# Optimization experiments

Hardware: AMD Instinct MI355X
Metric: run time of the kernel (lower is better)

Reference implementation:

```python
import jax, jax.numpy as jnp
import numpy as np

D_MODEL, D_K, D_V = 1024, 64, 64
B, S = 2, 4096
NEG = 1e9


def setup_inputs() -> dict:
    key = jax.random.key(0)
    ks = jax.random.split(key, 10)
    Q = jax.random.normal(ks[0], (B, S, D_MODEL), dtype=jnp.float32)
    K = jax.random.normal(ks[1], (B, S, D_MODEL), dtype=jnp.float32)
    V = jax.random.normal(ks[2], (B, S, D_MODEL), dtype=jnp.float32)
    mask = jax.random.randint(ks[3], (B, S, S), 0, 2, dtype=jnp.int32)
    sc = 1.0 / np.sqrt(D_MODEL)
    Wq = jax.random.normal(ks[4], (D_K, D_MODEL), dtype=jnp.float32) * sc
    bq = jnp.zeros((D_K,), dtype=jnp.float32)
    Wk = jax.random.normal(ks[5], (D_K, D_MODEL), dtype=jnp.float32) * sc
    bk = jnp.zeros((D_K,), dtype=jnp.float32)
    Wv = jax.random.normal(ks[6], (D_V, D_MODEL), dtype=jnp.float32) * sc
    bv = jnp.zeros((D_V,), dtype=jnp.float32)
    return {"Q": Q, "K": K, "V": V, "mask": mask,
            "Wq": Wq, "bq": bq, "Wk": Wk, "bk": bk, "Wv": Wv, "bv": bv}


def reference(Q, K, V, mask, Wq, bq, Wk, bk, Wv, bv):
    # Linear projections: q,k -> [B,S,d_k], v -> [B,S,d_v]
    q = jnp.einsum('bsm,km->bsk', Q, Wq) + bq
    k = jnp.einsum('bsm,km->bsk', K, Wk) + bk
    v = jnp.einsum('bsm,vm->bsv', V, Wv) + bv
    # Scaled dot-product scores [B,S,S]
    x = jnp.einsum('bqk,bsk->bqs', q, k) / jnp.sqrt(jnp.float32(D_K))
    m = mask.astype(x.dtype)
    x = x * m - NEG * (1.0 - m)
    x = jax.nn.softmax(x, axis=2)
    y = jnp.einsum('bqs,bsv->bqv', x, v)
    return y
```

## Files before the change

### kernel.cpp

```cpp
#include <hip/hip_runtime.h>

typedef unsigned short u16;
typedef unsigned long long u64;
typedef __bf16 bf16x8 __attribute__((ext_vector_type(8)));
typedef float f32x4 __attribute__((ext_vector_type(4)));
typedef int i32x4 __attribute__((ext_vector_type(4)));

#define MFMA16(a, b, c) __builtin_amdgcn_mfma_f32_16x16x32_bf16((a), (b), (c), 0, 0, 0)

__device__ __forceinline__ bf16x8 ld8(const u16* p) {
    return *reinterpret_cast<const bf16x8*>(p);
}

__device__ __forceinline__ unsigned pk2(float a, float b) {
    unsigned short ua = __builtin_bit_cast(unsigned short, (__bf16)a);
    unsigned short ub = __builtin_bit_cast(unsigned short, (__bf16)b);
    return (unsigned)ua | ((unsigned)ub << 16);
}

__device__ __forceinline__ f32x4 ntf4(const float* p) {
    return __builtin_nontemporal_load(reinterpret_cast<const f32x4*>(p));
}
__device__ __forceinline__ i32x4 nti4(const int* p) {
    return __builtin_nontemporal_load(reinterpret_cast<const i32x4*>(p));
}

__global__ __launch_bounds__(256) void wcvt_kernel(
    const float* __restrict__ Wq, const float* __restrict__ Wk,
    const float* __restrict__ Wv, u16* __restrict__ wb)
{
    const int t = blockIdx.x * 256 + threadIdx.x;
    const int mat = t >> 13;
    const int idx = (t & 8191) * 8;
    const float* src = (mat == 0) ? Wq : (mat == 1) ? Wk : Wv;
    const f32x4 a = *(const f32x4*)(src + idx);
    const f32x4 b = *(const f32x4*)(src + idx + 4);
    uint4 o;
    o.x = pk2(a[0], a[1]); o.y = pk2(a[2], a[3]);
    o.z = pk2(b[0], b[1]); o.w = pk2(b[2], b[3]);
    *reinterpret_cast<uint4*>(wb + (size_t)mat * 65536 + idx) = o;
}

__global__ __launch_bounds__(256) void fused_kernel(
    const float* __restrict__ Q, const float* __restrict__ K, const float* __restrict__ V,
    const float* __restrict__ bq, const float* __restrict__ bk, const float* __restrict__ bv,
    const u16* __restrict__ wb, const int* __restrict__ mask,
    u16* __restrict__ qb, u16* __restrict__ kb, u16* __restrict__ vtb,
    u64* __restrict__ bits)
{
    __shared__ uint2 xlds[16][256];
    const int lane = threadIdx.x & 63, w = threadIdx.x >> 6;

    if (blockIdx.x >= 1536) {
        const int row = (blockIdx.x - 1536) * 4 + w;
        const int* mp = mask + (size_t)row * 4096 + lane * 4;
        u64* op = bits + (size_t)row * 64;

        i32x4 h0[8], h1[8];
        #pragma unroll
        for (int j = 0; j < 8; ++j) h0[j] = nti4(mp + j * 256);
        #pragma unroll
        for (int j = 0; j < 8; ++j) h1[j] = nti4(mp + 2048 + j * 256);

        u64 mine0 = 0, mine1 = 0;
        #pragma unroll
        for (int j = 0; j < 8; ++j) {
            const u64 b0 = __ballot(h0[j][0] != 0);
            const u64 b1 = __ballot(h0[j][1] != 0);
            const u64 b2 = __ballot(h0[j][2] != 0);
            const u64 b3 = __ballot(h0[j][3] != 0);
            if (lane == j * 4 + 0) mine0 = b0;
            if (lane == j * 4 + 1) mine0 = b1;
            if (lane == j * 4 + 2) mine0 = b2;
            if (lane == j * 4 + 3) mine0 = b3;
            const u64 c0 = __ballot(h1[j][0] != 0);
            const u64 c1 = __ballot(h1[j][1] != 0);
            const u64 c2 = __ballot(h1[j][2] != 0);
            const u64 c3 = __ballot(h1[j][3] != 0);
            if (lane == j * 4 + 0) mine1 = c0;
            if (lane == j * 4 + 1) mine1 = c1;
            if (lane == j * 4 + 2) mine1 = c2;
            if (lane == j * 4 + 3) mine1 = c3;
        }
        if (lane < 32) { op[lane] = mine0; op[32 + lane] = mine1; }
        return;
    }

    const int mat  = blockIdx.x >> 9;
    const int tile = blockIdx.x & 511;
    const int r0   = tile * 16;
    const int t    = threadIdx.x;
    const float* X = (mat == 0) ? Q : (mat == 1) ? K : V;

    f32x4 st[16];
    const float* xp = X + (size_t)r0 * 1024 + t * 4;
    #pragma unroll
    for (int i = 0; i < 16; ++i) st[i] = ntf4(xp + i * 1024);

    #pragma unroll
    for (int i = 0; i < 16; ++i) {
        xlds[i][(((t >> 1) ^ (i & 7)) << 1) | (t & 1)] =
            make_uint2(pk2(st[i][0], st[i][1]), pk2(st[i][2], st[i][3]));
    }
    __syncthreads();

    const int c = lane & 15, g = lane >> 4;
    const u16* wp = wb + (size_t)mat * 65536 + (size_t)(w * 16 + c) * 1024 + g * 8;

    f32x4 acc = {};
    #pragma unroll
    for (int kk = 0; kk < 32; ++kk) {
        const bf16x8 a = ld8((const u16*)&xlds[c][((kk * 4 + g) ^ (c & 7)) << 1]);
        const bf16x8 wf = ld8(wp + kk * 32);
        if (mat < 2) acc = MFMA16(a, wf, acc);
        else         acc = MFMA16(wf, a, acc);
    }

    if (mat < 2) {
        const float* bias = (mat == 0) ? bq : bk;
        u16* dst = (mat == 0) ? qb : kb;
        const float bz = bias[w * 16 + c];
        #pragma unroll
        for (int r = 0; r < 4; ++r) {
            dst[(size_t)(r0 + g * 4 + r) * 64 + w * 16 + c] =
                __builtin_bit_cast(u16, (__bf16)(acc[r] + bz));
        }
    } else {
        const int sg = r0 + c;
        const int bidx = sg >> 12, sin = sg & 4095;
        #pragma unroll
        for (int r = 0; r < 4; ++r) {
            const int dv = w * 16 + g * 4 + r;
            vtb[(size_t)(bidx * 64 + dv) * 4096 + sin] =
                __builtin_bit_cast(u16, (__bf16)(acc[r] + bv[dv]));
        }
    }
}

__global__ __launch_bounds__(256) void attn_kernel(
    const u64* __restrict__ bits, const u16* __restrict__ qb,
    const u16* __restrict__ kb, const u16* __restrict__ vtb,
    float* __restrict__ pacc, float* __restrict__ pm, float* __restrict__ pl)
{
    __shared__ uint2 plds[4][128];
    const int lane = threadIdx.x & 63, w = threadIdx.x >> 6;
    const int c = lane & 15, g = lane >> 4;
    const int gw    = blockIdx.x * 4 + w;
    const int strip = gw >> 3;
    const int chunk = gw & 7;
    const int b     = strip >> 8;
    const int q0    = (strip & 255) * 16;
    const int sBase = chunk * 512;
    const float SSC = 0.18033688011112042f;

    const u16* qrow = qb + (size_t)((b << 12) + q0 + c) * 64 + g * 8;
    const bf16x8 qf0 = ld8(qrow);
    const bf16x8 qf1 = ld8(qrow + 32);

    const u16* kfp = kb  + (((size_t)b << 12) + sBase + c) * 64 + g * 8;
    const u16* vfp = vtb + (size_t)(b * 64 + c) * 4096 + sBase + g * 8;

    const u64* bp = bits + (size_t)((b << 12) + q0 + c) * 64 + chunk * 8;
    const u64 Wd0 = bp[0], Wd1 = bp[1], Wd2 = bp[2], Wd3 = bp[3];
    const u64 Wd4 = bp[4], Wd5 = bp[5], Wd6 = bp[6], Wd7 = bp[7];

    f32x4 acc0 = {}, acc1 = {}, acc2 = {}, acc3 = {};
    const f32x4 zf = {};
    float m_run = -__builtin_inff(), l_run = 0.f;

    bf16x8 k00 = ld8(kfp),            k01 = ld8(kfp + 32);
    bf16x8 k10 = ld8(kfp + 16 * 64),  k11 = ld8(kfp + 16 * 64 + 32);

    #pragma unroll
    for (int half = 0; half < 2; ++half) {
        const u64 Wr0 = half ? Wd4 : Wd0;
        const u64 Wr1 = half ? Wd5 : Wd1;
        const u64 Wr2 = half ? Wd6 : Wd2;
        const u64 Wr3 = half ? Wd7 : Wd3;
        #pragma unroll 1
        for (int it2 = 0; it2 < 8; ++it2) {
            const int it = half * 8 + it2;

            const u16* vp = vfp + it * 32;
            const bf16x8 v0 = ld8(vp);
            const bf16x8 v1 = ld8(vp + 16 * 4096);
            const bf16x8 v2 = ld8(vp + 32 * 4096);
            const bf16x8 v3 = ld8(vp + 48 * 4096);

            f32x4 d0 = MFMA16(k00, qf0, zf);
            d0 = MFMA16(k01, qf1, d0);
            f32x4 d1 = MFMA16(k10, qf0, zf);
            d1 = MFMA16(k11, qf1, d1);

            const int no = (it < 15) ? (it + 1) * 2048 : it * 2048;
            k00 = ld8(kfp + no);            k01 = ld8(kfp + no + 32);
            k10 = ld8(kfp + no + 16 * 64);  k11 = ld8(kfp + no + 16 * 64 + 32);

            const int sh = it2 * 8 + g;
            const unsigned t0 = (unsigned)(Wr0 >> sh);
            const unsigned t1 = (unsigned)(Wr1 >> sh);
            const unsigned t2 = (unsigned)(Wr2 >> sh);
            const unsigned t3 = (unsigned)(Wr3 >> sh);

            const float x0 = (t0 & 1u)  ? d0[0] * SSC : -1e9f;
            const float x1 = (t1 & 1u)  ? d0[1] * SSC : -1e9f;
            const float x2 = (t2 & 1u)  ? d0[2] * SSC : -1e9f;
            const float x3 = (t3 & 1u)  ? d0[3] * SSC : -1e9f;
            const float x4 = (t0 & 16u) ? d1[0] * SSC : -1e9f;
            const float x5 = (t1 & 16u) ? d1[1] * SSC : -1e9f;
            const float x6 = (t2 & 16u) ? d1[2] * SSC : -1e9f;
            const float x7 = (t3 & 16u) ? d1[3] * SSC : -1e9f;

            float tm = fmaxf(fmaxf(fmaxf(x0, x1), fmaxf(x2, x3)),
                             fmaxf(fmaxf(x4, x5), fmaxf(x6, x7)));
            tm = fmaxf(tm, __shfl_xor(tm, 16));
            tm = fmaxf(tm, __shfl_xor(tm, 32));
            const float m_new = fmaxf(m_run, tm);
            const float f = exp2f(m_run - m_new);

            const float p0 = exp2f(x0 - m_new), p1 = exp2f(x1 - m_new);
            const float p2 = exp2f(x2 - m_new), p3 = exp2f(x3 - m_new);
            const float p4 = exp2f(x4 - m_new), p5 = exp2f(x5 - m_new);
            const float p6 = exp2f(x6 - m_new), p7 = exp2f(x7 - m_new);
            float rs = ((p0 + p1) + (p2 + p3)) + ((p4 + p5) + (p6 + p7));
            rs += __shfl_xor(rs, 16);
            rs += __shfl_xor(rs, 32);
            l_run = l_run * f + rs;
            m_run = m_new;

            plds[w][c * 8 + ( g      ^ (c & 7))] = make_uint2(pk2(p0, p1), pk2(p2, p3));
            plds[w][c * 8 + ((g + 4) ^ (c & 7))] = make_uint2(pk2(p4, p5), pk2(p6, p7));

            if (__any(f < 1.0f)) {
                const float f0 = __shfl(f, g * 4 + 0);
                const float f1 = __shfl(f, g * 4 + 1);
                const float f2 = __shfl(f, g * 4 + 2);
                const float f3 = __shfl(f, g * 4 + 3);
                acc0[0] *= f0; acc0[1] *= f1; acc0[2] *= f2; acc0[3] *= f3;
                acc1[0] *= f0; acc1[1] *= f1; acc1[2] *= f2; acc1[3] *= f3;
                acc2[0] *= f0; acc2[1] *= f1; acc2[2] *= f2; acc2[3] *= f3;
                acc3[0] *= f0; acc3[1] *= f1; acc3[2] *= f2; acc3[3] *= f3;
            }

            union { uint2 u[2]; bf16x8 v; } pa;
            pa.u[0] = plds[w][c * 8 + ((2 * g    ) ^ (c & 7))];
            pa.u[1] = plds[w][c * 8 + ((2 * g + 1) ^ (c & 7))];

            acc0 = MFMA16(pa.v, v0, acc0);
            acc1 = MFMA16(pa.v, v1, acc1);
            acc2 = MFMA16(pa.v, v2, acc2);
            acc3 = MFMA16(pa.v, v3, acc3);
        }
    }

    const size_t pidx = (size_t)(strip * 8 + chunk) * 16;
    #pragma unroll
    for (int r = 0; r < 4; ++r) {
        const size_t row = pidx + g * 4 + r;
        pacc[row * 64 +  0 + c] = acc0[r];
        pacc[row * 64 + 16 + c] = acc1[r];
        pacc[row * 64 + 32 + c] = acc2[r];
        pacc[row * 64 + 48 + c] = acc3[r];
    }
    if (lane < 16) {
        pm[pidx + c] = m_run;
        pl[pidx + c] = l_run;
    }
}

__global__ __launch_bounds__(256) void comb_kernel(
    const float* __restrict__ pacc, const float* __restrict__ pm,
    const float* __restrict__ pl, float* __restrict__ out)
{
    const int t = blockIdx.x * 256 + threadIdx.x;
    const int r = t >> 6, dv = t & 63;
    const int strip = r >> 4, qi = r & 15;
    const int base = strip * 128 + qi;
    float mv[8];
    float M = -__builtin_inff();
    #pragma unroll
    for (int cc = 0; cc < 8; ++cc) { mv[cc] = pm[base + cc * 16]; M = fmaxf(M, mv[cc]); }
    float num = 0.f, den = 0.f;
    #pragma unroll
    for (int cc = 0; cc < 8; ++cc) {
        const float wgt = exp2f(mv[cc] - M);
        num += wgt * pacc[(size_t)(base + cc * 16) * 64 + dv];
        den += wgt * pl[base + cc * 16];
    }
    out[t] = num / den;
}

extern "C" void kernel_launch(void* const* d_in, const int* in_sizes, int n_in,
                              void* d_out, int out_size, void* d_ws, size_t ws_size,
                              hipStream_t stream)
{
    const float* Q    = (const float*)d_in[0];
    const float* K    = (const float*)d_in[1];
    const float* V    = (const float*)d_in[2];
    const int*   mask = (const int*)d_in[3];
    const float* Wq   = (const float*)d_in[4];
    const float* bq   = (const float*)d_in[5];
    const float* Wk   = (const float*)d_in[6];
    const float* bk   = (const float*)d_in[7];
    const float* Wv   = (const float*)d_in[8];
    const float* bv   = (const float*)d_in[9];
    float* out = (float*)d_out;

    char* ws = (char*)d_ws;
    u16*   wb   = (u16*)(ws);
    u16*   qb   = (u16*)(ws + 393216);
    u16*   kb   = (u16*)(ws + 393216 + 1048576);
    u16*   vtb  = (u16*)(ws + 393216 + 2097152);
    u64*   bits = (u64*)(ws + 4194304);
    float* pm   = (float*)(ws + 8388608);
    float* pl   = (float*)(ws + 8388608 + 262144);
    float* pacc = (float*)(ws + 8388608 + 524288);

    wcvt_kernel<<<96, 256, 0, stream>>>(Wq, Wk, Wv, wb);
    fused_kernel<<<3584, 256, 0, stream>>>(Q, K, V, bq, bk, bv, wb, mask,
                                           qb, kb, vtb, bits);
    attn_kernel<<<1024, 256, 0, stream>>>(bits, qb, kb, vtb, pacc, pm, pl);
    comb_kernel<<<2048, 256, 0, stream>>>(pacc, pm, pl, out);
}
```

Measured before the change: 133.8 us.

## Split projection K-dimension into two halves with software-pipelined loads

The projection phase now stages each 16-row input tile into shared memory in two 512-column halves instead of all at once. The second half's global loads are issued before the MFMA loop over the first half, so memory latency overlaps with compute. Shared memory per block is halved, which may improve occupancy, at the cost of two extra barriers.

New measurement: 143.7 us. 1.07x slower.

```diff
diff --git a/kernel.cpp b/kernel.cpp
--- a/kernel.cpp
+++ b/kernel.cpp
@@ -48,7 +48,7 @@
     u16* __restrict__ qb, u16* __restrict__ kb, u16* __restrict__ vtb,
     u64* __restrict__ bits)
 {
-    __shared__ uint2 xlds[16][256];
+    __shared__ uint2 xlds[16][128];
     const int lane = threadIdx.x & 63, w = threadIdx.x >> 6;
 
     if (blockIdx.x >= 1536) {
@@ -90,28 +90,51 @@
     const int tile = blockIdx.x & 511;
     const int r0   = tile * 16;
     const int t    = threadIdx.x;
+    const int trow = t >> 7;
+    const int tcol = t & 127;
     const float* X = (mat == 0) ? Q : (mat == 1) ? K : V;
 
-    f32x4 st[16];
-    const float* xp = X + (size_t)r0 * 1024 + t * 4;
-    #pragma unroll
-    for (int i = 0; i < 16; ++i) st[i] = ntf4(xp + i * 1024);
-
-    #pragma unroll
-    for (int i = 0; i < 16; ++i) {
-        xlds[i][(((t >> 1) ^ (i & 7)) << 1) | (t & 1)] =
-            make_uint2(pk2(st[i][0], st[i][1]), pk2(st[i][2], st[i][3]));
-    }
-    __syncthreads();
+    const float* xb = X + (size_t)r0 * 1024 + (size_t)trow * 1024 + tcol * 4;
 
     const int c = lane & 15, g = lane >> 4;
     const u16* wp = wb + (size_t)mat * 65536 + (size_t)(w * 16 + c) * 1024 + g * 8;
-
     f32x4 acc = {};
-    #pragma unroll
-    for (int kk = 0; kk < 32; ++kk) {
-        const bf16x8 a = ld8((const u16*)&xlds[c][((kk * 4 + g) ^ (c & 7)) << 1]);
-        const bf16x8 wf = ld8(wp + kk * 32);
+
+    f32x4 st[8];
+    #pragma unroll
+    for (int j = 0; j < 8; ++j) st[j] = ntf4(xb + j * 2048);
+    #pragma unroll
+    for (int j = 0; j < 8; ++j) {
+        const int i = j * 2 + trow;
+        xlds[i][((((tcol >> 1) ^ (i & 7)) << 1) | (tcol & 1))] =
+            make_uint2(pk2(st[j][0], st[j][1]), pk2(st[j][2], st[j][3]));
+    }
+    __syncthreads();
+
+    f32x4 st2[8];
+    #pragma unroll
+    for (int j = 0; j < 8; ++j) st2[j] = ntf4(xb + j * 2048 + 512);
+
+    #pragma unroll
+    for (int kkl = 0; kkl < 16; ++kkl) {
+        const bf16x8 a = ld8((const u16*)&xlds[c][((kkl * 4 + g) ^ (c & 7)) << 1]);
+        const bf16x8 wf = ld8(wp + kkl * 32);
+        if (mat < 2) acc = MFMA16(a, wf, acc);
+        else         acc = MFMA16(wf, a, acc);
+    }
+    __syncthreads();
+
+    #pragma unroll
+    for (int j = 0; j < 8; ++j) {
+        const int i = j * 2 + trow;
+        xlds[i][((((tcol >> 1) ^ (i & 7)) << 1) | (tcol & 1))] =
+            make_uint2(pk2(st2[j][0], st2[j][1]), pk2(st2[j][2], st2[j][3]));
+    }
+    __syncthreads();
+    #pragma unroll
+    for (int kkl = 0; kkl < 16; ++kkl) {
+        const bf16x8 a = ld8((const u16*)&xlds[c][((kkl * 4 + g) ^ (c & 7)) << 1]);
+        const bf16x8 wf = ld8(wp + (16 + kkl) * 32);
         if (mat < 2) acc = MFMA16(a, wf, acc);
         else         acc = MFMA16(wf, a, acc);
     }
```

## Fuse split-KV combine into attention kernel via per-strip atomic counter

Applied to the files above, without the earlier changes.

Removes the separate combine kernel. Each attention block fences its partial results and atomically increments a per-strip counter. The second block to finish a strip merges all eight chunk partials and writes the final output. The counters are zeroed by block 0 of the earlier fused kernel. This drops one kernel launch and its pipeline gap, and reads the partials while they are likely still in L2. In exchange it adds a fence, an atomic and a tail of combine work to the attention kernel.

Result: slower. 335.0 us (+150.4%).

```diff
diff --git a/kernel.cpp b/kernel.cpp
--- a/kernel.cpp
+++ b/kernel.cpp
@@ -46,10 +46,15 @@
     const float* __restrict__ bq, const float* __restrict__ bk, const float* __restrict__ bv,
     const u16* __restrict__ wb, const int* __restrict__ mask,
     u16* __restrict__ qb, u16* __restrict__ kb, u16* __restrict__ vtb,
-    u64* __restrict__ bits)
+    u64* __restrict__ bits, unsigned* __restrict__ cnt)
 {
     __shared__ uint2 xlds[16][256];
     const int lane = threadIdx.x & 63, w = threadIdx.x >> 6;
+
+    if (blockIdx.x == 0) {
+        cnt[threadIdx.x] = 0;
+        cnt[256 + threadIdx.x] = 0;
+    }
 
     if (blockIdx.x >= 1536) {
         const int row = (blockIdx.x - 1536) * 4 + w;
@@ -140,9 +145,11 @@
 __global__ __launch_bounds__(256) void attn_kernel(
     const u64* __restrict__ bits, const u16* __restrict__ qb,
     const u16* __restrict__ kb, const u16* __restrict__ vtb,
-    float* __restrict__ pacc, float* __restrict__ pm, float* __restrict__ pl)
+    float* __restrict__ pacc, float* __restrict__ pm, float* __restrict__ pl,
+    unsigned* __restrict__ cnt, float* __restrict__ out)
 {
     __shared__ uint2 plds[4][128];
+    __shared__ unsigned sdone;
     const int lane = threadIdx.x & 63, w = threadIdx.x >> 6;
     const int c = lane & 15, g = lane >> 4;
     const int gw    = blockIdx.x * 4 + w;
@@ -266,28 +273,33 @@
         pm[pidx + c] = m_run;
         pl[pidx + c] = l_run;
     }
-}
-
-__global__ __launch_bounds__(256) void comb_kernel(
-    const float* __restrict__ pacc, const float* __restrict__ pm,
-    const float* __restrict__ pl, float* __restrict__ out)
-{
-    const int t = blockIdx.x * 256 + threadIdx.x;
-    const int r = t >> 6, dv = t & 63;
-    const int strip = r >> 4, qi = r & 15;
-    const int base = strip * 128 + qi;
-    float mv[8];
-    float M = -__builtin_inff();
-    #pragma unroll
-    for (int cc = 0; cc < 8; ++cc) { mv[cc] = pm[base + cc * 16]; M = fmaxf(M, mv[cc]); }
-    float num = 0.f, den = 0.f;
-    #pragma unroll
-    for (int cc = 0; cc < 8; ++cc) {
-        const float wgt = exp2f(mv[cc] - M);
-        num += wgt * pacc[(size_t)(base + cc * 16) * 64 + dv];
-        den += wgt * pl[base + cc * 16];
-    }
-    out[t] = num / den;
+
+    __threadfence();
+    __syncthreads();
+    if (threadIdx.x == 0) sdone = atomicAdd(&cnt[strip], 1u);
+    __syncthreads();
+    if (sdone != 1u) return;
+    __threadfence();
+
+    const int sb = strip * 8;
+    #pragma unroll
+    for (int e4 = 0; e4 < 4; ++e4) {
+        const int e  = e4 * 256 + threadIdx.x;
+        const int qi = e >> 6, dv = e & 63;
+        const int base = sb * 16 + qi;
+        float mv[8];
+        float M = -__builtin_inff();
+        #pragma unroll
+        for (int cc = 0; cc < 8; ++cc) { mv[cc] = pm[base + cc * 16]; M = fmaxf(M, mv[cc]); }
+        float num = 0.f, den = 0.f;
+        #pragma unroll
+        for (int cc = 0; cc < 8; ++cc) {
+            const float wgt = exp2f(mv[cc] - M);
+            num += wgt * pacc[(size_t)(base + cc * 16) * 64 + dv];
+            den += wgt * pl[base + cc * 16];
+        }
+        out[(size_t)(strip * 16 + qi) * 64 + dv] = num / den;
+    }
 }
 
 extern "C" void kernel_launch(void* const* d_in, const int* in_sizes, int n_in,
@@ -315,10 +327,10 @@
     float* pm   = (float*)(ws + 8388608);
     float* pl   = (float*)(ws + 8388608 + 262144);
     float* pacc = (float*)(ws + 8388608 + 524288);
+    unsigned* cnt = (unsigned*)(ws + 8388608 + 524288 + 16777216);
 
     wcvt_kernel<<<96, 256, 0, stream>>>(Wq, Wk, Wv, wb);
     fused_kernel<<<3584, 256, 0, stream>>>(Q, K, V, bq, bk, bv, wb, mask,
-                                           qb, kb, vtb, bits);
-    attn_kernel<<<1024, 256, 0, stream>>>(bits, qb, kb, vtb, pacc, pm, pl);
-    comb_kernel<<<2048, 256, 0, stream>>>(pacc, pm, pl, out);
-}
+                                           qb, kb, vtb, bits, cnt);
+    attn_kernel<<<1024, 256, 0, stream>>>(bits, qb, kb, vtb, pacc, pm, pl, cnt, out);
+}
```
